# Performance work log

Measured on AMD Instinct MI355X. Metric: run time of the kernel, lower is better.

The kernel has to match this reference:

```python
import jax, jax.numpy as jnp
import numpy as np


def setup_inputs() -> dict:
    key = jax.random.key(0)
    k1, k2, k3 = jax.random.split(key, 3)
    B, M, J = 4096, 64, 24  # batch, n_max_markers, n_joints
    points = jax.random.normal(k1, (B, M, 3), dtype=jnp.float32)
    weight = jax.random.uniform(k2, (B, M, J), dtype=jnp.float32)  # positive soft weights
    offset = jax.random.normal(k3, (B, M, J, 3), dtype=jnp.float32)
    return {"points": points, "weight": weight, "offset": offset}


def reference(points, weight, offset):
    # P: per-joint marker offsets (B, J, 3, M); Q: world marker positions (B, 1, 3, M)
    P = jnp.transpose(offset, (0, 2, 3, 1))
    Q = jnp.transpose(points, (0, 2, 1))[:, None]
    w = jnp.transpose(weight, (0, 2, 1))[:, :, None]  # (B, J, 1, M)

    wsum = jnp.sum(w, axis=-1)                   # (B, J, 1)
    P_ = jnp.sum(P * w, axis=-1) / wsum          # (B, J, 3) weighted centroid of offsets
    Q_ = jnp.sum(Q * w, axis=-1) / wsum          # (B, J, 3) weighted centroid of markers

    X = P - P_[..., None]                        # (B, J, 3, M)
    Y = Q - Q_[..., None]                        # (B, J, 3, M) via broadcast

    # Cross-covariance S = X @ Y^T (NOTE: original multiplies un-weighted centered coords)
    S = jnp.einsum('bjdm,bjem->bjde', X, Y)      # (B, J, 3, 3)

    U, _, Vh = jnp.linalg.svd(S)
    V = jnp.swapaxes(Vh, -1, -2)
    Ut = jnp.swapaxes(U, -1, -2)
    det = jnp.linalg.det(jnp.matmul(V, Ut))      # (B, J) reflection correction
    Ut = Ut.at[..., -1, :].multiply(det[..., None])
    R = jnp.matmul(V, Ut)                        # (B, J, 3, 3) optimal rotation
    t = Q_[..., None] - jnp.matmul(R, P_[..., None])  # (B, J, 3, 1)
    return R, t
```

## Files before the change

### kernel.cpp

```cpp
#include <hip/hip_runtime.h>


constexpr int M = 64;
constexpr int J = 24;
constexpr int NACC = 22;

constexpr int LW = 0;
constexpr int LO = 1536;
constexpr int LP = 6144;
constexpr int LTOT = 6336;

__global__ __launch_bounds__(256) void accum_kernel(
    const float* __restrict__ points,
    const float* __restrict__ weight,
    const float* __restrict__ offset,
    float* __restrict__ ws,
    int bj_total)
{
    __shared__ float smem[LTOT];
    const int t = threadIdx.x;
    const int b = blockIdx.x;

    float4* s4 = (float4*)smem;
    const float4* wg4 = (const float4*)(weight + (size_t)b * (M * J));
    const float4* og4 = (const float4*)(offset + (size_t)b * (M * J * 3));
    const float4* pg4 = (const float4*)(points + (size_t)b * (M * 3));
#pragma unroll
    for (int i = 0; i < 2; ++i) {
        int idx = t + i * 256;
        if (idx < 384) s4[LW / 4 + idx] = wg4[idx];
    }
#pragma unroll
    for (int i = 0; i < 5; ++i) {
        int idx = t + i * 256;
        if (idx < 1152) s4[LO / 4 + idx] = og4[idx];
    }
    if (t < 48) s4[LP / 4 + t] = pg4[t];

    __syncthreads();

    if (t >= 192) return;
    const int j = t >> 3;
    const int k = t & 7;

    float acc[NACC];
#pragma unroll
    for (int n = 0; n < NACC; ++n) acc[n] = 0.0f;

#pragma unroll
    for (int ii = 0; ii < M / 8; ++ii) {
        const int i = (ii + k) & 7;
        const int m = k * 8 + i;
        float w  = smem[LW + m * 24 + j];
        float o0 = smem[LO + m * 72 + j * 3 + 0];
        float o1 = smem[LO + m * 72 + j * 3 + 1];
        float o2 = smem[LO + m * 72 + j * 3 + 2];
        float p0 = smem[LP + m * 3 + 0];
        float p1 = smem[LP + m * 3 + 1];
        float p2 = smem[LP + m * 3 + 2];
        acc[0] += w;
        acc[1] = fmaf(w, o0, acc[1]);  acc[2] = fmaf(w, o1, acc[2]);  acc[3] = fmaf(w, o2, acc[3]);
        acc[4] = fmaf(w, p0, acc[4]);  acc[5] = fmaf(w, p1, acc[5]);  acc[6] = fmaf(w, p2, acc[6]);
        acc[7] += o0; acc[8] += o1; acc[9] += o2;
        acc[10] += p0; acc[11] += p1; acc[12] += p2;
        acc[13] = fmaf(o0, p0, acc[13]); acc[14] = fmaf(o0, p1, acc[14]); acc[15] = fmaf(o0, p2, acc[15]);
        acc[16] = fmaf(o1, p0, acc[16]); acc[17] = fmaf(o1, p1, acc[17]); acc[18] = fmaf(o1, p2, acc[18]);
        acc[19] = fmaf(o2, p0, acc[19]); acc[20] = fmaf(o2, p1, acc[20]); acc[21] = fmaf(o2, p2, acc[21]);
    }

#pragma unroll
    for (int n = 0; n < NACC; ++n) {
        float v = acc[n];
        v += __shfl_xor(v, 1);
        v += __shfl_xor(v, 2);
        v += __shfl_xor(v, 4);
        acc[n] = v;
    }

    if (k != 0) return;

    const float inv = __builtin_amdgcn_rcpf(acc[0]);
    const float cP0 = acc[1] * inv, cP1 = acc[2] * inv, cP2 = acc[3] * inv;
    const float cQ0 = acc[4] * inv, cQ1 = acc[5] * inv, cQ2 = acc[6] * inv;
    const float To0 = acc[7], To1 = acc[8], To2 = acc[9];
    const float Tp0 = acc[10], Tp1 = acc[11], Tp2 = acc[12];
    const float fM = (float)M;
    float4 f0, f1, f2, f3;
    f0.x = acc[13] - cP0 * Tp0 - cQ0 * To0 + fM * cP0 * cQ0;
    f0.y = acc[14] - cP0 * Tp1 - cQ1 * To0 + fM * cP0 * cQ1;
    f0.z = acc[15] - cP0 * Tp2 - cQ2 * To0 + fM * cP0 * cQ2;
    f0.w = acc[16] - cP1 * Tp0 - cQ0 * To1 + fM * cP1 * cQ0;
    f1.x = acc[17] - cP1 * Tp1 - cQ1 * To1 + fM * cP1 * cQ1;
    f1.y = acc[18] - cP1 * Tp2 - cQ2 * To1 + fM * cP1 * cQ2;
    f1.z = acc[19] - cP2 * Tp0 - cQ0 * To2 + fM * cP2 * cQ0;
    f1.w = acc[20] - cP2 * Tp1 - cQ1 * To2 + fM * cP2 * cQ1;
    f2.x = acc[21] - cP2 * Tp2 - cQ2 * To2 + fM * cP2 * cQ2;
    f2.y = cP0; f2.z = cP1; f2.w = cP2;
    f3.x = cQ0; f3.y = cQ1; f3.z = cQ2; f3.w = 0.0f;

    const int bj = b * J + j;
    float4* dst = (float4*)(ws + (size_t)bj * 16);
    dst[0] = f0; dst[1] = f1; dst[2] = f2; dst[3] = f3;
}

template<int P, int Q>
__device__ __forceinline__ void jrot(float A[4][4], float V[4][4]) {
    float apq = A[P][Q];
    float theta = (A[Q][Q] - A[P][P]) * __builtin_amdgcn_rcpf(2.0f * apq);
    float t = __builtin_amdgcn_rcpf(fabsf(theta) + __builtin_amdgcn_sqrtf(fmaf(theta, theta, 1.0f)));
    t = (theta < 0.0f) ? -t : t;
    t = (apq == 0.0f) ? 0.0f : t;
    float c = __builtin_amdgcn_rsqf(fmaf(t, t, 1.0f));
    float s = t * c;
#pragma unroll
    for (int k = 0; k < 4; ++k) {
        float akp = A[k][P], akq = A[k][Q];
        A[k][P] = c * akp - s * akq;
        A[k][Q] = s * akp + c * akq;
    }
#pragma unroll
    for (int k = 0; k < 4; ++k) {
        float apk = A[P][k], aqk = A[Q][k];
        A[P][k] = c * apk - s * aqk;
        A[Q][k] = s * apk + c * aqk;
        float vkp = V[k][P], vkq = V[k][Q];
        V[k][P] = c * vkp - s * vkq;
        V[k][Q] = s * vkp + c * vkq;
    }
}

__device__ __forceinline__ void horn_solve(
    float S00, float S01, float S02, float S10, float S11, float S12,
    float S20, float S21, float S22,
    float cP0, float cP1, float cP2, float cQ0, float cQ1, float cQ2,
    float* __restrict__ Rout, float* __restrict__ tout)
{
    float A[4][4], V[4][4];
    A[0][0] = S00 + S11 + S22;
    A[0][1] = A[1][0] = S12 - S21;
    A[0][2] = A[2][0] = S20 - S02;
    A[0][3] = A[3][0] = S01 - S10;
    A[1][1] = S00 - S11 - S22;
    A[1][2] = A[2][1] = S01 + S10;
    A[1][3] = A[3][1] = S02 + S20;
    A[2][2] = -S00 + S11 - S22;
    A[2][3] = A[3][2] = S12 + S21;
    A[3][3] = -S00 - S11 + S22;
#pragma unroll
    for (int r = 0; r < 4; ++r)
#pragma unroll
        for (int c = 0; c < 4; ++c)
            V[r][c] = (r == c) ? 1.0f : 0.0f;

#pragma unroll 1
    for (int sweep = 0; sweep < 6; ++sweep) {
        jrot<0, 1>(A, V); jrot<0, 2>(A, V); jrot<0, 3>(A, V);
        jrot<1, 2>(A, V); jrot<1, 3>(A, V); jrot<2, 3>(A, V);
    }

    float best = A[0][0];
    float qw = V[0][0], qx = V[1][0], qy = V[2][0], qz = V[3][0];
#pragma unroll
    for (int i = 1; i < 4; ++i) {
        bool better = A[i][i] > best;
        best = better ? A[i][i] : best;
        qw = better ? V[0][i] : qw;
        qx = better ? V[1][i] : qx;
        qy = better ? V[2][i] : qy;
        qz = better ? V[3][i] : qz;
    }
    float nrm = __builtin_amdgcn_rsqf(qw * qw + qx * qx + qy * qy + qz * qz);
    qw *= nrm; qx *= nrm; qy *= nrm; qz *= nrm;

    float R00 = 1.f - 2.f * (qy * qy + qz * qz);
    float R01 = 2.f * (qx * qy - qw * qz);
    float R02 = 2.f * (qx * qz + qw * qy);
    float R10 = 2.f * (qx * qy + qw * qz);
    float R11 = 1.f - 2.f * (qx * qx + qz * qz);
    float R12 = 2.f * (qy * qz - qw * qx);
    float R20 = 2.f * (qx * qz - qw * qy);
    float R21 = 2.f * (qy * qz + qw * qx);
    float R22 = 1.f - 2.f * (qx * qx + qy * qy);

    Rout[0] = R00; Rout[1] = R01; Rout[2] = R02;
    Rout[3] = R10; Rout[4] = R11; Rout[5] = R12;
    Rout[6] = R20; Rout[7] = R21; Rout[8] = R22;
    tout[0] = cQ0 - (R00 * cP0 + R01 * cP1 + R02 * cP2);
    tout[1] = cQ1 - (R10 * cP0 + R11 * cP1 + R12 * cP2);
    tout[2] = cQ2 - (R20 * cP0 + R21 * cP1 + R22 * cP2);
}

__global__ __launch_bounds__(256) void solve_kernel(
    const float* __restrict__ ws, float* __restrict__ out, int bj_total)
{
    int tid = blockIdx.x * 256 + threadIdx.x;
    if (tid >= bj_total) return;
    const float4* v = (const float4*)(ws + (size_t)tid * 16);
    float4 f0 = v[0], f1 = v[1], f2 = v[2], f3 = v[3];
    float Rr[9], tr[3];
    horn_solve(f0.x, f0.y, f0.z, f0.w, f1.x, f1.y, f1.z, f1.w, f2.x,
               f2.y, f2.z, f2.w, f3.x, f3.y, f3.z, Rr, tr);
    float* Rout = out + (size_t)tid * 9;
#pragma unroll
    for (int n = 0; n < 9; ++n) Rout[n] = Rr[n];
    float* tout = out + (size_t)bj_total * 9 + (size_t)tid * 3;
    tout[0] = tr[0]; tout[1] = tr[1]; tout[2] = tr[2];
}

__global__ __launch_bounds__(256) void fused_kernel(
    const float* __restrict__ points, const float* __restrict__ weight,
    const float* __restrict__ offset, float* __restrict__ out, int bj_total)
{
    int tid = blockIdx.x * blockDim.x + threadIdx.x;
    if (tid >= bj_total) return;
    int b = tid / J, j = tid - b * J;
    const float* wq = weight + (size_t)b * M * J + j;
    const float* oq = offset + ((size_t)b * M * J + j) * 3;
    const float* pq = points + (size_t)b * M * 3;
    float a[NACC];
#pragma unroll
    for (int n = 0; n < NACC; ++n) a[n] = 0.0f;
#pragma unroll 4
    for (int m = 0; m < M; ++m) {
        float w = wq[m * J];
        float o0 = oq[m * (J * 3) + 0], o1 = oq[m * (J * 3) + 1], o2 = oq[m * (J * 3) + 2];
        float p0 = pq[m * 3 + 0], p1 = pq[m * 3 + 1], p2 = pq[m * 3 + 2];
        a[0] += w;
        a[1] = fmaf(w, o0, a[1]); a[2] = fmaf(w, o1, a[2]); a[3] = fmaf(w, o2, a[3]);
        a[4] = fmaf(w, p0, a[4]); a[5] = fmaf(w, p1, a[5]); a[6] = fmaf(w, p2, a[6]);
        a[7] += o0; a[8] += o1; a[9] += o2;
        a[10] += p0; a[11] += p1; a[12] += p2;
        a[13] = fmaf(o0, p0, a[13]); a[14] = fmaf(o0, p1, a[14]); a[15] = fmaf(o0, p2, a[15]);
        a[16] = fmaf(o1, p0, a[16]); a[17] = fmaf(o1, p1, a[17]); a[18] = fmaf(o1, p2, a[18]);
        a[19] = fmaf(o2, p0, a[19]); a[20] = fmaf(o2, p1, a[20]); a[21] = fmaf(o2, p2, a[21]);
    }
    float inv = __builtin_amdgcn_rcpf(a[0]);
    float cP0 = a[1] * inv, cP1 = a[2] * inv, cP2 = a[3] * inv;
    float cQ0 = a[4] * inv, cQ1 = a[5] * inv, cQ2 = a[6] * inv;
    const float fM = (float)M;
    float S00 = a[13] - cP0 * a[10] - cQ0 * a[7] + fM * cP0 * cQ0;
    float S01 = a[14] - cP0 * a[11] - cQ1 * a[7] + fM * cP0 * cQ1;
    float S02 = a[15] - cP0 * a[12] - cQ2 * a[7] + fM * cP0 * cQ2;
    float S10 = a[16] - cP1 * a[10] - cQ0 * a[8] + fM * cP1 * cQ0;
    float S11 = a[17] - cP1 * a[11] - cQ1 * a[8] + fM * cP1 * cQ1;
    float S12 = a[18] - cP1 * a[12] - cQ2 * a[8] + fM * cP1 * cQ2;
    float S20 = a[19] - cP2 * a[10] - cQ0 * a[9] + fM * cP2 * cQ0;
    float S21 = a[20] - cP2 * a[11] - cQ1 * a[9] + fM * cP2 * cQ1;
    float S22 = a[21] - cP2 * a[12] - cQ2 * a[9] + fM * cP2 * cQ2;
    float Rr[9], tr[3];
    horn_solve(S00, S01, S02, S10, S11, S12, S20, S21, S22,
               cP0, cP1, cP2, cQ0, cQ1, cQ2, Rr, tr);
    float* Rout = out + (size_t)tid * 9;
#pragma unroll
    for (int n = 0; n < 9; ++n) Rout[n] = Rr[n];
    float* tout = out + (size_t)bj_total * 9 + (size_t)tid * 3;
    tout[0] = tr[0]; tout[1] = tr[1]; tout[2] = tr[2];
}

extern "C" void kernel_launch(void* const* d_in, const int* in_sizes, int n_in,
                              void* d_out, int out_size, void* d_ws, size_t ws_size,
                              hipStream_t stream) {
    const float* points = (const float*)d_in[0];
    const float* weight = (const float*)d_in[1];
    const float* offset = (const float*)d_in[2];
    float* out = (float*)d_out;

    int B = in_sizes[0] / (M * 3);
    int bj_total = B * J;

    size_t need = (size_t)bj_total * 16 * sizeof(float);
    if (ws_size >= need) {
        accum_kernel<<<B, 256, 0, stream>>>(points, weight, offset, (float*)d_ws, bj_total);
        solve_kernel<<<(bj_total + 255) / 256, 256, 0, stream>>>((const float*)d_ws, out, bj_total);
    } else {
        fused_kernel<<<(bj_total + 255) / 256, 256, 0, stream>>>(points, weight, offset, out, bj_total);
    }
}
```

Before: 151.0 us.

## Double-buffer async global-to-LDS loads across several batches per block

The accumulation kernel now handles four batch elements per block. It stages each element's weight, offset and points into a double-buffered LDS area using global_load_lds DMA, prefetching the next batch while the current one is reduced. The aim is to hide global-memory latency behind the reduction and to cut the number of blocks launched. In exchange it doubles LDS use per block and reduces grid parallelism. It also depends on the barrier waiting for the asynchronous LDS writes to finish.

```diff
diff --git a/kernel.cpp b/kernel.cpp
--- a/kernel.cpp
+++ b/kernel.cpp
@@ -9,98 +9,121 @@
 constexpr int LO = 1536;
 constexpr int LP = 6144;
 constexpr int LTOT = 6336;
+constexpr int GPB = 4;
+
+__device__ __forceinline__ void chunk_async(const float* src, float* dst, int lane) {
+    __builtin_amdgcn_global_load_lds(
+        (const __attribute__((address_space(1))) void*)(src + lane * 4),
+        (__attribute__((address_space(3))) void*)dst, 16, 0, 0);
+}
+
+__device__ __forceinline__ void stage_batch(
+    const float* __restrict__ w, const float* __restrict__ o,
+    const float* __restrict__ p, float* buf, int wv, int lane)
+{
+#pragma unroll
+    for (int c = wv; c < 25; c += 4) {
+        if (c < 6) {
+            chunk_async(w + c * 256, buf + LW + c * 256, lane);
+        } else if (c < 24) {
+            chunk_async(o + (c - 6) * 256, buf + LO + (c - 6) * 256, lane);
+        } else if (lane < 48) {
+            chunk_async(p, buf + LP, lane);
+        }
+    }
+}
 
 __global__ __launch_bounds__(256) void accum_kernel(
     const float* __restrict__ points,
     const float* __restrict__ weight,
     const float* __restrict__ offset,
     float* __restrict__ ws,
-    int bj_total)
-{
-    __shared__ float smem[LTOT];
-    const int t = threadIdx.x;
-    const int b = blockIdx.x;
-
-    float4* s4 = (float4*)smem;
-    const float4* wg4 = (const float4*)(weight + (size_t)b * (M * J));
-    const float4* og4 = (const float4*)(offset + (size_t)b * (M * J * 3));
-    const float4* pg4 = (const float4*)(points + (size_t)b * (M * 3));
-#pragma unroll
-    for (int i = 0; i < 2; ++i) {
-        int idx = t + i * 256;
-        if (idx < 384) s4[LW / 4 + idx] = wg4[idx];
-    }
-#pragma unroll
-    for (int i = 0; i < 5; ++i) {
-        int idx = t + i * 256;
-        if (idx < 1152) s4[LO / 4 + idx] = og4[idx];
-    }
-    if (t < 48) s4[LP / 4 + t] = pg4[t];
-
-    __syncthreads();
-
-    if (t >= 192) return;
+    int B, int bj_total)
+{
+    __shared__ float smem[2 * LTOT];
+    const int t    = threadIdx.x;
+    const int lane = t & 63;
+    const int wv   = t >> 6;
+    const int b0   = blockIdx.x * GPB;
+
+    if (b0 < B)
+        stage_batch(weight + (size_t)b0 * (M * J), offset + (size_t)b0 * (M * J * 3),
+                    points + (size_t)b0 * (M * 3), smem, wv, lane);
+
     const int j = t >> 3;
     const int k = t & 7;
 
-    float acc[NACC];
-#pragma unroll
-    for (int n = 0; n < NACC; ++n) acc[n] = 0.0f;
-
-#pragma unroll
-    for (int ii = 0; ii < M / 8; ++ii) {
-        const int i = (ii + k) & 7;
-        const int m = k * 8 + i;
-        float w  = smem[LW + m * 24 + j];
-        float o0 = smem[LO + m * 72 + j * 3 + 0];
-        float o1 = smem[LO + m * 72 + j * 3 + 1];
-        float o2 = smem[LO + m * 72 + j * 3 + 2];
-        float p0 = smem[LP + m * 3 + 0];
-        float p1 = smem[LP + m * 3 + 1];
-        float p2 = smem[LP + m * 3 + 2];
-        acc[0] += w;
-        acc[1] = fmaf(w, o0, acc[1]);  acc[2] = fmaf(w, o1, acc[2]);  acc[3] = fmaf(w, o2, acc[3]);
-        acc[4] = fmaf(w, p0, acc[4]);  acc[5] = fmaf(w, p1, acc[5]);  acc[6] = fmaf(w, p2, acc[6]);
-        acc[7] += o0; acc[8] += o1; acc[9] += o2;
-        acc[10] += p0; acc[11] += p1; acc[12] += p2;
-        acc[13] = fmaf(o0, p0, acc[13]); acc[14] = fmaf(o0, p1, acc[14]); acc[15] = fmaf(o0, p2, acc[15]);
-        acc[16] = fmaf(o1, p0, acc[16]); acc[17] = fmaf(o1, p1, acc[17]); acc[18] = fmaf(o1, p2, acc[18]);
-        acc[19] = fmaf(o2, p0, acc[19]); acc[20] = fmaf(o2, p1, acc[20]); acc[21] = fmaf(o2, p2, acc[21]);
-    }
-
-#pragma unroll
-    for (int n = 0; n < NACC; ++n) {
-        float v = acc[n];
-        v += __shfl_xor(v, 1);
-        v += __shfl_xor(v, 2);
-        v += __shfl_xor(v, 4);
-        acc[n] = v;
-    }
-
-    if (k != 0) return;
-
-    const float inv = __builtin_amdgcn_rcpf(acc[0]);
-    const float cP0 = acc[1] * inv, cP1 = acc[2] * inv, cP2 = acc[3] * inv;
-    const float cQ0 = acc[4] * inv, cQ1 = acc[5] * inv, cQ2 = acc[6] * inv;
-    const float To0 = acc[7], To1 = acc[8], To2 = acc[9];
-    const float Tp0 = acc[10], Tp1 = acc[11], Tp2 = acc[12];
-    const float fM = (float)M;
-    float4 f0, f1, f2, f3;
-    f0.x = acc[13] - cP0 * Tp0 - cQ0 * To0 + fM * cP0 * cQ0;
-    f0.y = acc[14] - cP0 * Tp1 - cQ1 * To0 + fM * cP0 * cQ1;
-    f0.z = acc[15] - cP0 * Tp2 - cQ2 * To0 + fM * cP0 * cQ2;
-    f0.w = acc[16] - cP1 * Tp0 - cQ0 * To1 + fM * cP1 * cQ0;
-    f1.x = acc[17] - cP1 * Tp1 - cQ1 * To1 + fM * cP1 * cQ1;
-    f1.y = acc[18] - cP1 * Tp2 - cQ2 * To1 + fM * cP1 * cQ2;
-    f1.z = acc[19] - cP2 * Tp0 - cQ0 * To2 + fM * cP2 * cQ0;
-    f1.w = acc[20] - cP2 * Tp1 - cQ1 * To2 + fM * cP2 * cQ1;
-    f2.x = acc[21] - cP2 * Tp2 - cQ2 * To2 + fM * cP2 * cQ2;
-    f2.y = cP0; f2.z = cP1; f2.w = cP2;
-    f3.x = cQ0; f3.y = cQ1; f3.z = cQ2; f3.w = 0.0f;
-
-    const int bj = b * J + j;
-    float4* dst = (float4*)(ws + (size_t)bj * 16);
-    dst[0] = f0; dst[1] = f1; dst[2] = f2; dst[3] = f3;
+#pragma unroll 1
+    for (int g = 0; g < GPB; ++g) {
+        __syncthreads();
+
+        if (g + 1 < GPB && b0 + g + 1 < B) {
+            const int bn = b0 + g + 1;
+            stage_batch(weight + (size_t)bn * (M * J), offset + (size_t)bn * (M * J * 3),
+                        points + (size_t)bn * (M * 3), smem + ((g + 1) & 1) * LTOT, wv, lane);
+        }
+
+        if (t < 192 && b0 + g < B) {
+            const float* buf = smem + (g & 1) * LTOT;
+            float acc[NACC];
+#pragma unroll
+            for (int n = 0; n < NACC; ++n) acc[n] = 0.0f;
+
+#pragma unroll
+            for (int ii = 0; ii < M / 8; ++ii) {
+                const int i = (ii + k) & 7;
+                const int m = k * 8 + i;
+                float w  = buf[LW + m * 24 + j];
+                float o0 = buf[LO + m * 72 + j * 3 + 0];
+                float o1 = buf[LO + m * 72 + j * 3 + 1];
+                float o2 = buf[LO + m * 72 + j * 3 + 2];
+                float p0 = buf[LP + m * 3 + 0];
+                float p1 = buf[LP + m * 3 + 1];
+                float p2 = buf[LP + m * 3 + 2];
+                acc[0] += w;
+                acc[1] = fmaf(w, o0, acc[1]);  acc[2] = fmaf(w, o1, acc[2]);  acc[3] = fmaf(w, o2, acc[3]);
+                acc[4] = fmaf(w, p0, acc[4]);  acc[5] = fmaf(w, p1, acc[5]);  acc[6] = fmaf(w, p2, acc[6]);
+                acc[7] += o0; acc[8] += o1; acc[9] += o2;
+                acc[10] += p0; acc[11] += p1; acc[12] += p2;
+                acc[13] = fmaf(o0, p0, acc[13]); acc[14] = fmaf(o0, p1, acc[14]); acc[15] = fmaf(o0, p2, acc[15]);
+                acc[16] = fmaf(o1, p0, acc[16]); acc[17] = fmaf(o1, p1, acc[17]); acc[18] = fmaf(o1, p2, acc[18]);
+                acc[19] = fmaf(o2, p0, acc[19]); acc[20] = fmaf(o2, p1, acc[20]); acc[21] = fmaf(o2, p2, acc[21]);
+            }
+
+#pragma unroll
+            for (int n = 0; n < NACC; ++n) {
+                float v = acc[n];
+                v += __shfl_xor(v, 1);
+                v += __shfl_xor(v, 2);
+                v += __shfl_xor(v, 4);
+                acc[n] = v;
+            }
+
+            if (k == 0) {
+                const float inv = __builtin_amdgcn_rcpf(acc[0]);
+                const float cP0 = acc[1] * inv, cP1 = acc[2] * inv, cP2 = acc[3] * inv;
+                const float cQ0 = acc[4] * inv, cQ1 = acc[5] * inv, cQ2 = acc[6] * inv;
+                const float To0 = acc[7], To1 = acc[8], To2 = acc[9];
+                const float Tp0 = acc[10], Tp1 = acc[11], Tp2 = acc[12];
+                const float fM = (float)M;
+                float4 f0, f1, f2, f3;
+                f0.x = acc[13] - cP0 * Tp0 - cQ0 * To0 + fM * cP0 * cQ0;
+                f0.y = acc[14] - cP0 * Tp1 - cQ1 * To0 + fM * cP0 * cQ1;
+                f0.z = acc[15] - cP0 * Tp2 - cQ2 * To0 + fM * cP0 * cQ2;
+                f0.w = acc[16] - cP1 * Tp0 - cQ0 * To1 + fM * cP1 * cQ0;
+                f1.x = acc[17] - cP1 * Tp1 - cQ1 * To1 + fM * cP1 * cQ1;
+                f1.y = acc[18] - cP1 * Tp2 - cQ2 * To1 + fM * cP1 * cQ2;
+                f1.z = acc[19] - cP2 * Tp0 - cQ0 * To2 + fM * cP2 * cQ0;
+                f1.w = acc[20] - cP2 * Tp1 - cQ1 * To2 + fM * cP2 * cQ1;
+                f2.x = acc[21] - cP2 * Tp2 - cQ2 * To2 + fM * cP2 * cQ2;
+                f2.y = cP0; f2.z = cP1; f2.w = cP2;
+                f3.x = cQ0; f3.y = cQ1; f3.z = cQ2; f3.w = 0.0f;
+                const int bj = (b0 + g) * J + j;
+                float4* dst = (float4*)(ws + (size_t)bj * 16);
+                dst[0] = f0; dst[1] = f1; dst[2] = f2; dst[3] = f3;
+            }
+        }
+    }
 }
 
 template<int P, int Q>
@@ -270,7 +293,8 @@
 
     size_t need = (size_t)bj_total * 16 * sizeof(float);
     if (ws_size >= need) {
-        accum_kernel<<<B, 256, 0, stream>>>(points, weight, offset, (float*)d_ws, bj_total);
+        int grid1 = (B + GPB - 1) / GPB;
+        accum_kernel<<<grid1, 256, 0, stream>>>(points, weight, offset, (float*)d_ws, B, bj_total);
         solve_kernel<<<(bj_total + 255) / 256, 256, 0, stream>>>((const float*)d_ws, out, bj_total);
     } else {
         fused_kernel<<<(bj_total + 255) / 256, 256, 0, stream>>>(points, weight, offset, out, bj_total);
```

Result: no change. 149.3 us (-1.1%).
